# Kernel optimization log

Hardware: AMD Instinct MI355X
Metric: run time of the kernel (lower is better)

## Reference

```python
import jax, jax.numpy as jnp
import numpy as np
from jax import lax

EPS = 1e-12  # F.normalize eps


def _l2norm(x, axis):
    n = jnp.sqrt(jnp.sum(x * x, axis=axis, keepdims=True))
    return x / jnp.maximum(n, EPS)


def setup_inputs() -> dict:
    key = jax.random.key(0)
    k1, k2 = jax.random.split(key)
    b, t, c, E = 4, 4096, 2048, 64
    return {
        "hidden_states": jax.random.normal(k1, (b, t, c), dtype=jnp.float32),
        "sim_matrix": jax.random.normal(k2, (c, E), dtype=jnp.float32),
        "gates": jnp.zeros((E,), dtype=jnp.float32),
        "fallback_k": 2,
    }


def reference(hidden_states, sim_matrix, gates, fallback_k):
    b, t, c = hidden_states.shape
    x = hidden_states.reshape(b * t, c)
    # normalized similarity logits: cosine(x, expert) - gate
    logits = jnp.matmul(_l2norm(x, -1), _l2norm(sim_matrix, 0)) - gates  # [N, E]
    gated = jax.nn.relu(logits)
    # STE: forward is hard {0,1}, backward is identity
    hard = (gated > 0).astype(gated.dtype)
    ste_mask = gated + lax.stop_gradient(hard - gated)
    inactive = jnp.sum(hard, axis=1) == 0  # [N] rows with no active expert
    # fallback: top-k of raw logits, computed for all rows (static shape), applied only to inactive rows
    _, top_idx = lax.top_k(logits, fallback_k)  # [N, k]
    n = logits.shape[0]
    fallback_mask = jnp.zeros_like(logits).at[jnp.arange(n)[:, None], top_idx].set(1.0)
    activation_mask = jnp.where(inactive[:, None], lax.stop_gradient(fallback_mask), ste_mask)
    masked = jnp.where(activation_mask > 0, gated, -jnp.inf)
    routing_weights = jax.nn.softmax(masked, axis=-1)
    return routing_weights, logits, activation_mask
```

## Files before the change

kernel.cpp:

```cpp
#include <hip/hip_runtime.h>
#include <hip/hip_bf16.h>
#include <math.h>

#define C_DIM 2048
#define E_DIM 64
#define KC 32
#define NCHUNK 64
#define KC_BLK 12

typedef __attribute__((address_space(3))) float lds_f;
typedef const __attribute__((address_space(1))) float glb_f;


__global__ __launch_bounds__(256) void xnorm_kernel(const float* __restrict__ X,
                                                    float* __restrict__ den, int N) {
  const int w = threadIdx.x >> 6, l = threadIdx.x & 63;
  const int row = blockIdx.x * 8 + w * 2 + (l >> 5);
  const int task = l & 31;
  const int b = task >> 1, a = (task & 1) * 4;
  const float* p0 = X + (size_t)row * C_DIM + b * 128 + a;

  float4 v = *(const float4*)p0;
  float ax = __fmul_rn(v.x, v.x), ay = __fmul_rn(v.y, v.y);
  float az = __fmul_rn(v.z, v.z), aw = __fmul_rn(v.w, v.w);
#pragma unroll
  for (int p = 1; p < 16; ++p) {
    v = *(const float4*)(p0 + p * 8);
    ax = __fadd_rn(ax, __fmul_rn(v.x, v.x));
    ay = __fadd_rn(ay, __fmul_rn(v.y, v.y));
    az = __fadd_rn(az, __fmul_rn(v.z, v.z));
    aw = __fadd_rn(aw, __fmul_rn(v.w, v.w));
  }
  float r = __fadd_rn(__fadd_rn(ax, ay), __fadd_rn(az, aw));
  r = __fadd_rn(r, __shfl_xor(r, 1));
  r = __fadd_rn(r, __shfl_xor(r, 2));
  r = __fadd_rn(r, __shfl_xor(r, 4));
  r = __fadd_rn(r, __shfl_xor(r, 8));
  r = __fadd_rn(r, __shfl_xor(r, 16));
  if (task == 0 && row < N) den[row] = fmaxf(sqrtf(r), 1e-12f);
}

__global__ __launch_bounds__(64) void simnorm_a_kernel(const float* __restrict__ sim,
                                                       float* __restrict__ Bsum) {
  const int b = blockIdx.x, l = threadIdx.x;
  const float* base = sim + (size_t)(b * 128) * E_DIM + l;
#define SQ(c) __fmul_rn(base[(c) * E_DIM], base[(c) * E_DIM])
  float a0 = SQ(0), a1 = SQ(1), a2 = SQ(2), a3 = SQ(3);
  float a4 = SQ(4), a5 = SQ(5), a6 = SQ(6), a7 = SQ(7);
#pragma unroll
  for (int g = 1; g < 16; ++g) {
    a0 = __fadd_rn(a0, SQ(g * 8 + 0)); a1 = __fadd_rn(a1, SQ(g * 8 + 1));
    a2 = __fadd_rn(a2, SQ(g * 8 + 2)); a3 = __fadd_rn(a3, SQ(g * 8 + 3));
    a4 = __fadd_rn(a4, SQ(g * 8 + 4)); a5 = __fadd_rn(a5, SQ(g * 8 + 5));
    a6 = __fadd_rn(a6, SQ(g * 8 + 6)); a7 = __fadd_rn(a7, SQ(g * 8 + 7));
  }
#undef SQ
  const float left = __fadd_rn(__fadd_rn(a0, a1), __fadd_rn(a2, a3));
  const float right = __fadd_rn(__fadd_rn(a4, a5), __fadd_rn(a6, a7));
  Bsum[b * E_DIM + l] = __fadd_rn(left, right);
}

__global__ __launch_bounds__(256) void simnorm_b_kernel(const float* __restrict__ sim,
                                                        const float* __restrict__ Bsum,
                                                        float* __restrict__ sT) {
  const int e = blockIdx.x, t = threadIdx.x;
  float B[16];
#pragma unroll
  for (int b = 0; b < 16; ++b) B[b] = Bsum[b * E_DIM + e];
  float c01 = __fadd_rn(B[0], B[1]), c23 = __fadd_rn(B[2], B[3]);
  float c45 = __fadd_rn(B[4], B[5]), c67 = __fadd_rn(B[6], B[7]);
  float c89 = __fadd_rn(B[8], B[9]), cab = __fadd_rn(B[10], B[11]);
  float ccd = __fadd_rn(B[12], B[13]), cef = __fadd_rn(B[14], B[15]);
  float q0 = __fadd_rn(c01, c23), q1 = __fadd_rn(c45, c67);
  float q2 = __fadd_rn(c89, cab), q3 = __fadd_rn(ccd, cef);
  const float tot = __fadd_rn(__fadd_rn(q0, q1), __fadd_rn(q2, q3));
  const float den = fmaxf(sqrtf(tot), 1e-12f);
#pragma unroll
  for (int i = 0; i < 8; ++i) {
    const int c = t + i * 256;
    sT[(size_t)e * C_DIM + c] = sim[(size_t)c * E_DIM + e] / den;
  }
}

__global__ __launch_bounds__(128) void gating_main(const float* __restrict__ X,
                                                   const float* __restrict__ denx,
                                                   const float* __restrict__ sT,
                                                   const float* __restrict__ gates,
                                                   const int* __restrict__ fbk,
                                                   float* __restrict__ out, int N) {
  __shared__ float smem[6144];
  const int t = threadIdx.x;
  const int we = t >> 6, l = t & 63;
  const int rg = l >> 3, eg = l & 7;
  const size_t rowbase = (size_t)blockIdx.x * 32;
  const float* Xb = X + rowbase * C_DIM;

  const int u0 = t, u1 = t + 128;
  const int r0 = u0 >> 3, cb0 = (u0 & 7) ^ ((r0 >> 2) & 7);
  const int r1 = u1 >> 3, cb1 = (u1 & 7) ^ ((r1 >> 2) & 7);
  const float d0 = denx[rowbase + r0];
  const float d1 = denx[rowbase + r1];
  const float* xg0 = Xb + (size_t)r0 * C_DIM + cb0 * 4;
  const float* xg1 = Xb + (size_t)r1 * C_DIM + cb1 * 4;

  const float* sg[4];
  int sdst[4];
#pragma unroll
  for (int it = 0; it < 4; ++it) {
    const int v = t + 128 * it;
    const int er = v >> 3, cb = (v & 7) ^ ((er >> 2) & 7);
    sg[it] = sT + (size_t)er * C_DIM + cb * 4;
    sdst[it] = 2048 + v * 4;
  }

  float4 xr0, xr1;
  auto issueX = [&](int ch) {
    xr0 = *(const float4*)(xg0 + ch * KC);
    xr1 = *(const float4*)(xg1 + ch * KC);
  };
  auto issueS = [&](int buf, int ch) {
#pragma unroll
    for (int it = 0; it < 4; ++it) {
      glb_f* g = (glb_f*)(sg[it] + ch * KC);
      lds_f* d = (lds_f*)&smem[sdst[it] + buf * 2048];
      __builtin_amdgcn_global_load_lds((const __attribute__((address_space(1))) void*)g,
                                       (__attribute__((address_space(3))) void*)d, 16, 0, 0);
    }
  };
  auto writeX = [&](int buf) {
    float4 a, b;
    a.x = xr0.x / d0; a.y = xr0.y / d0; a.z = xr0.z / d0; a.w = xr0.w / d0;
    b.x = xr1.x / d1; b.y = xr1.y / d1; b.z = xr1.z / d1; b.w = xr1.w / d1;
    *(float4*)&smem[buf * 1024 + u0 * 4] = a;
    *(float4*)&smem[buf * 1024 + u1 * 4] = b;
  };

  float ab[4][4], tt[4][4];
#pragma unroll
  for (int i = 0; i < 4; ++i)
#pragma unroll
    for (int j = 0; j < 4; ++j) ab[i][j] = 0.f;

  issueX(0);
  issueS(0, 0);
  writeX(0);
  asm volatile("s_waitcnt vmcnt(0) lgkmcnt(0)" ::: "memory");
  __builtin_amdgcn_s_barrier();
  asm volatile("" ::: "memory");

  for (int ch = 0; ch < NCHUNK; ++ch) {
    const int buf = ch & 1;
    if (ch + 1 < NCHUNK) {
      issueX(ch + 1);
      issueS(buf ^ 1, ch + 1);
    }
    if (ch && (ch % KC_BLK) == 0) {
#pragma unroll
      for (int i = 0; i < 4; ++i)
#pragma unroll
        for (int j = 0; j < 4; ++j) {
          if (ch == KC_BLK) tt[i][j] = ab[i][j];
          else tt[i][j] = __fadd_rn(tt[i][j], ab[i][j]);
          ab[i][j] = 0.f;
        }
    }

    const int xb = buf * 1024;
    const int sb = 2048 + buf * 2048;
#pragma unroll
    for (int u = 0; u < 8; ++u) {
      float4 xv[4], sv[4];
#pragma unroll
      for (int i = 0; i < 4; ++i) {
        const int row = rg * 4 + i;
        xv[i] = *(const float4*)&smem[xb + row * 32 + ((u ^ rg) * 4)];
      }
#pragma unroll
      for (int j = 0; j < 4; ++j) {
        const int er = we * 32 + eg * 4 + j;
        sv[j] = *(const float4*)&smem[sb + er * 32 + ((u ^ eg) * 4)];
      }
#pragma unroll
      for (int i = 0; i < 4; ++i)
#pragma unroll
        for (int j = 0; j < 4; ++j) {
          float a = ab[i][j];
          a = fmaf(xv[i].x, sv[j].x, a);
          a = fmaf(xv[i].y, sv[j].y, a);
          a = fmaf(xv[i].z, sv[j].z, a);
          a = fmaf(xv[i].w, sv[j].w, a);
          ab[i][j] = a;
        }
    }
    asm volatile("" ::: "memory");
    if (ch + 1 < NCHUNK) writeX(buf ^ 1);
    asm volatile("s_waitcnt vmcnt(0) lgkmcnt(0)" ::: "memory");
    __builtin_amdgcn_s_barrier();
    asm volatile("" ::: "memory");
  }
#pragma unroll
  for (int i = 0; i < 4; ++i)
#pragma unroll
    for (int j = 0; j < 4; ++j) tt[i][j] = __fadd_rn(tt[i][j], ab[i][j]);

  float* lg = smem;
#pragma unroll
  for (int i = 0; i < 4; ++i) {
    const int row = rg * 4 + i;
#pragma unroll
    for (int j = 0; j < 4; ++j) lg[row * 66 + we * 32 + eg * 4 + j] = tt[i][j];
  }
  __syncthreads();

  const int k = fbk[0];
  const float gate = gates[l];
  const size_t NE = (size_t)N * E_DIM;

  for (int rr = 0; rr < 16; ++rr) {
    const int row = we * 16 + rr;
    const float logit = __fadd_rn(lg[row * 66 + l], -gate);
    const float gated = fmaxf(logit, 0.f);
    const bool act = logit > 0.f;
    const unsigned long long bal = __ballot(act);
    const bool inactive = (bal == 0ull);

    float cur = logit;
    bool fb = false;
    for (int tk = 0; tk < k; ++tk) {
      float v2 = cur;
      int idx = l;
#pragma unroll
      for (int off = 32; off >= 1; off >>= 1) {
        const float ov = __shfl_xor(v2, off);
        const int oi = __shfl_xor(idx, off);
        if (ov > v2 || (ov == v2 && oi < idx)) { v2 = ov; idx = oi; }
      }
      if (l == idx) { cur = -INFINITY; fb = true; }
    }

    const float mask = inactive ? (fb ? 1.f : 0.f) : (act ? 1.f : 0.f);
    const float masked = (mask > 0.f) ? gated : -INFINITY;
    float m = masked;
#pragma unroll
    for (int off = 32; off >= 1; off >>= 1) m = fmaxf(m, __shfl_xor(m, off));
    const float p = (mask > 0.f) ? expf(masked - m) : 0.f;
    float s = p;
#pragma unroll
    for (int off = 32; off >= 1; off >>= 1) s += __shfl_xor(s, off);
    const float wgt = p / s;

    const size_t gr = rowbase + row;
    out[gr * E_DIM + l] = wgt;
    out[NE + gr * E_DIM + l] = logit;
    out[2 * NE + gr * E_DIM + l] = mask;
  }
}

extern "C" void kernel_launch(void* const* d_in, const int* in_sizes, int n_in,
                              void* d_out, int out_size, void* d_ws, size_t ws_size,
                              hipStream_t stream) {
  (void)n_in; (void)out_size; (void)ws_size;
  const float* X = (const float*)d_in[0];
  const float* sim = (const float*)d_in[1];
  const float* gates = (const float*)d_in[2];
  const int* fbk = (const int*)d_in[3];
  float* out = (float*)d_out;
  float* den = (float*)d_ws;
  float* sT = (float*)d_ws + 16384;
  float* Bsum = (float*)d_ws + 16384 + 131072;
  const int N = in_sizes[0] / C_DIM;

  hipLaunchKernelGGL(xnorm_kernel, dim3(N / 8), dim3(256), 0, stream, X, den, N);
  hipLaunchKernelGGL(simnorm_a_kernel, dim3(16), dim3(64), 0, stream, sim, Bsum);
  hipLaunchKernelGGL(simnorm_b_kernel, dim3(E_DIM), dim3(256), 0, stream, sim, Bsum, sT);
  hipLaunchKernelGGL(gating_main, dim3(N / 32), dim3(128), 0, stream, X, den, sT, gates, fbk, out, N);
}
```

Measured before the change: 353.2 us.

## Split K dimension across two wave pairs in gating GEMM block

Doubles the block to 256 threads and splits the 2048-wide reduction into two halves (36 and 28 chunks), each handled by a pair of waves with its own LDS double buffers. The partial sums are combined through shared memory in an order that reproduces the original blocked summation sequence. The epilogue then processes 8 rows per wave instead of 16. The aim is to shorten the per-block serial K loop and add latency hiding, at the cost of doubled LDS use, an uneven split, and extra reduction and sync work.

```diff
diff --git a/kernel.cpp b/kernel.cpp
--- a/kernel.cpp
+++ b/kernel.cpp
@@ -5,8 +5,7 @@
 #define C_DIM 2048
 #define E_DIM 64
 #define KC 32
-#define NCHUNK 64
-#define KC_BLK 12
+#define ITERS 36
 
 typedef __attribute__((address_space(3))) float lds_f;
 typedef const __attribute__((address_space(1))) float glb_f;
@@ -82,20 +81,27 @@
   }
 }
 
-__global__ __launch_bounds__(128) void gating_main(const float* __restrict__ X,
+__global__ __launch_bounds__(256) void gating_main(const float* __restrict__ X,
                                                    const float* __restrict__ denx,
                                                    const float* __restrict__ sT,
                                                    const float* __restrict__ gates,
                                                    const int* __restrict__ fbk,
                                                    float* __restrict__ out, int N) {
-  __shared__ float smem[6144];
+  __shared__ float smem[12288];
   const int t = threadIdx.x;
-  const int we = t >> 6, l = t & 63;
+  const int w = t >> 6, l = t & 63;
+  const int kh = w >> 1, we = w & 1;
   const int rg = l >> 3, eg = l & 7;
+  const int tg = t & 127;
   const size_t rowbase = (size_t)blockIdx.x * 32;
   const float* Xb = X + rowbase * C_DIM;
 
-  const int u0 = t, u1 = t + 128;
+  const int XB = kh * 2048;
+  const int SB = 4096 + kh * 4096;
+  const int KOFF = kh * 36;
+  const int LIM = kh ? 28 : 36;
+
+  const int u0 = tg, u1 = tg + 128;
   const int r0 = u0 >> 3, cb0 = (u0 & 7) ^ ((r0 >> 2) & 7);
   const int r1 = u1 >> 3, cb1 = (u1 & 7) ^ ((r1 >> 2) & 7);
   const float d0 = denx[rowbase + r0];
@@ -107,10 +113,10 @@
   int sdst[4];
 #pragma unroll
   for (int it = 0; it < 4; ++it) {
-    const int v = t + 128 * it;
+    const int v = tg + 128 * it;
     const int er = v >> 3, cb = (v & 7) ^ ((er >> 2) & 7);
     sg[it] = sT + (size_t)er * C_DIM + cb * 4;
-    sdst[it] = 2048 + v * 4;
+    sdst[it] = SB + v * 4;
   }
 
   float4 xr0, xr1;
@@ -131,84 +137,118 @@
     float4 a, b;
     a.x = xr0.x / d0; a.y = xr0.y / d0; a.z = xr0.z / d0; a.w = xr0.w / d0;
     b.x = xr1.x / d1; b.y = xr1.y / d1; b.z = xr1.z / d1; b.w = xr1.w / d1;
-    *(float4*)&smem[buf * 1024 + u0 * 4] = a;
-    *(float4*)&smem[buf * 1024 + u1 * 4] = b;
+    *(float4*)&smem[XB + buf * 1024 + u0 * 4] = a;
+    *(float4*)&smem[XB + buf * 1024 + u1 * 4] = b;
   };
 
-  float ab[4][4], tt[4][4];
+  float ab[4][4], A[4][4], B[4][4];
 #pragma unroll
   for (int i = 0; i < 4; ++i)
 #pragma unroll
-    for (int j = 0; j < 4; ++j) ab[i][j] = 0.f;
-
-  issueX(0);
-  issueS(0, 0);
+    for (int j = 0; j < 4; ++j) { ab[i][j] = 0.f; A[i][j] = 0.f; B[i][j] = 0.f; }
+
+  issueX(KOFF);
+  issueS(0, KOFF);
   writeX(0);
   asm volatile("s_waitcnt vmcnt(0) lgkmcnt(0)" ::: "memory");
   __builtin_amdgcn_s_barrier();
   asm volatile("" ::: "memory");
 
-  for (int ch = 0; ch < NCHUNK; ++ch) {
-    const int buf = ch & 1;
-    if (ch + 1 < NCHUNK) {
-      issueX(ch + 1);
-      issueS(buf ^ 1, ch + 1);
-    }
-    if (ch && (ch % KC_BLK) == 0) {
+  for (int it = 0; it < ITERS; ++it) {
+    const int buf = it & 1;
+    const bool nv = (it + 1) < LIM;
+    if (nv) {
+      issueX(KOFF + it + 1);
+      issueS(buf ^ 1, KOFF + it + 1);
+    }
+    if (it == 12) {
 #pragma unroll
       for (int i = 0; i < 4; ++i)
 #pragma unroll
+        for (int j = 0; j < 4; ++j) { A[i][j] = ab[i][j]; ab[i][j] = 0.f; }
+    }
+    if (it == 24) {
+#pragma unroll
+      for (int i = 0; i < 4; ++i)
+#pragma unroll
         for (int j = 0; j < 4; ++j) {
-          if (ch == KC_BLK) tt[i][j] = ab[i][j];
-          else tt[i][j] = __fadd_rn(tt[i][j], ab[i][j]);
+          if (kh == 0) A[i][j] = __fadd_rn(A[i][j], ab[i][j]);
+          else B[i][j] = ab[i][j];
           ab[i][j] = 0.f;
         }
     }
 
-    const int xb = buf * 1024;
-    const int sb = 2048 + buf * 2048;
-#pragma unroll
-    for (int u = 0; u < 8; ++u) {
-      float4 xv[4], sv[4];
-#pragma unroll
-      for (int i = 0; i < 4; ++i) {
-        const int row = rg * 4 + i;
-        xv[i] = *(const float4*)&smem[xb + row * 32 + ((u ^ rg) * 4)];
+    if (kh == 0 || it < 28) {
+      const int xb = XB + buf * 1024;
+      const int sb = SB + buf * 2048;
+#pragma unroll
+      for (int u = 0; u < 8; ++u) {
+        float4 xv[4], sv[4];
+#pragma unroll
+        for (int i = 0; i < 4; ++i) {
+          const int row = rg * 4 + i;
+          xv[i] = *(const float4*)&smem[xb + row * 32 + ((u ^ rg) * 4)];
+        }
+#pragma unroll
+        for (int j = 0; j < 4; ++j) {
+          const int er = we * 32 + eg * 4 + j;
+          sv[j] = *(const float4*)&smem[sb + er * 32 + ((u ^ eg) * 4)];
+        }
+#pragma unroll
+        for (int i = 0; i < 4; ++i)
+#pragma unroll
+          for (int j = 0; j < 4; ++j) {
+            float a = ab[i][j];
+            a = fmaf(xv[i].x, sv[j].x, a);
+            a = fmaf(xv[i].y, sv[j].y, a);
+            a = fmaf(xv[i].z, sv[j].z, a);
+            a = fmaf(xv[i].w, sv[j].w, a);
+            ab[i][j] = a;
+          }
       }
-#pragma unroll
-      for (int j = 0; j < 4; ++j) {
-        const int er = we * 32 + eg * 4 + j;
-        sv[j] = *(const float4*)&smem[sb + er * 32 + ((u ^ eg) * 4)];
-      }
-#pragma unroll
-      for (int i = 0; i < 4; ++i)
-#pragma unroll
-        for (int j = 0; j < 4; ++j) {
-          float a = ab[i][j];
-          a = fmaf(xv[i].x, sv[j].x, a);
-          a = fmaf(xv[i].y, sv[j].y, a);
-          a = fmaf(xv[i].z, sv[j].z, a);
-          a = fmaf(xv[i].w, sv[j].w, a);
-          ab[i][j] = a;
-        }
     }
     asm volatile("" ::: "memory");
-    if (ch + 1 < NCHUNK) writeX(buf ^ 1);
+    if (nv) writeX(buf ^ 1);
     asm volatile("s_waitcnt vmcnt(0) lgkmcnt(0)" ::: "memory");
     __builtin_amdgcn_s_barrier();
     asm volatile("" ::: "memory");
   }
-#pragma unroll
-  for (int i = 0; i < 4; ++i)
-#pragma unroll
-    for (int j = 0; j < 4; ++j) tt[i][j] = __fadd_rn(tt[i][j], ab[i][j]);
-
-  float* lg = smem;
-#pragma unroll
-  for (int i = 0; i < 4; ++i) {
-    const int row = rg * 4 + i;
-#pragma unroll
-    for (int j = 0; j < 4; ++j) lg[row * 66 + we * 32 + eg * 4 + j] = tt[i][j];
+  if (kh == 0) {
+#pragma unroll
+    for (int i = 0; i < 4; ++i)
+#pragma unroll
+      for (int j = 0; j < 4; ++j) A[i][j] = __fadd_rn(A[i][j], ab[i][j]);
+  }
+
+  if (kh == 1) {
+#pragma unroll
+    for (int i = 0; i < 4; ++i) {
+      const int row = rg * 4 + i;
+#pragma unroll
+      for (int j = 0; j < 4; ++j) {
+        const int e = we * 32 + eg * 4 + j;
+        smem[row * 66 + e] = A[i][j];
+        smem[2112 + row * 66 + e] = B[i][j];
+        smem[4224 + row * 66 + e] = ab[i][j];
+      }
+    }
+  }
+  __syncthreads();
+  float* lg = smem + 6400;
+  if (kh == 0) {
+#pragma unroll
+    for (int i = 0; i < 4; ++i) {
+      const int row = rg * 4 + i;
+#pragma unroll
+      for (int j = 0; j < 4; ++j) {
+        const int e = we * 32 + eg * 4 + j;
+        float v = A[i][j];
+        v = __fadd_rn(v, smem[row * 66 + e]);
+        v = __fadd_rn(v, smem[2112 + row * 66 + e]);
+        v = __fadd_rn(v, smem[4224 + row * 66 + e]);
+        lg[row * 66 + e] = v;
+      }
+    }
   }
   __syncthreads();
 
@@ -216,8 +256,8 @@
   const float gate = gates[l];
   const size_t NE = (size_t)N * E_DIM;
 
-  for (int rr = 0; rr < 16; ++rr) {
-    const int row = we * 16 + rr;
+  for (int rr = 0; rr < 8; ++rr) {
+    const int row = w * 8 + rr;
     const float logit = __fadd_rn(lg[row * 66 + l], -gate);
     const float gated = fmaxf(logit, 0.f);
     const bool act = logit > 0.f;
@@ -273,5 +313,5 @@
   hipLaunchKernelGGL(xnorm_kernel, dim3(N / 8), dim3(256), 0, stream, X, den, N);
   hipLaunchKernelGGL(simnorm_a_kernel, dim3(16), dim3(64), 0, stream, sim, Bsum);
   hipLaunchKernelGGL(simnorm_b_kernel, dim3(E_DIM), dim3(256), 0, stream, sim, Bsum, sT);
-  hipLaunchKernelGGL(gating_main, dim3(N / 32), dim3(128), 0, stream, X, den, sT, gates, fbk, out, N);
-}
+  hipLaunchKernelGGL(gating_main, dim3(N / 32), dim3(256), 0, stream, X, den, sT, gates, fbk, out, N);
+}
```

Measured after the change: 328.6 us. -7.0%, faster.
